# Kernel optimization log

Hardware: AMD Instinct MI355X
Metric: run time of the kernel (lower is better)

## Reference

```python
import jax, jax.numpy as jnp
import numpy as np

SIZE = 1024
SIZE_INTERNAL = 4096
B, S = 8, 2048
EPS = 1e-5


def layer_norm(x, g, b):
    mu = jnp.mean(x, axis=-1, keepdims=True)
    var = jnp.mean(jnp.square(x - mu), axis=-1, keepdims=True)
    return (x - mu) * jax.lax.rsqrt(var + EPS) * g + b


def setup_inputs() -> dict:
    key = jax.random.key(0)
    ks = jax.random.split(key, 12)
    s = 0.02
    return {
        "x": jax.random.normal(ks[0], (B, S, SIZE), jnp.float32),
        "Wq": jax.random.normal(ks[1], (SIZE, SIZE), jnp.float32) * s,
        "bq": jnp.zeros((SIZE,), jnp.float32),
        "Wk": jax.random.normal(ks[2], (SIZE, SIZE), jnp.float32) * s,
        "bk": jnp.zeros((SIZE,), jnp.float32),
        "Wv": jax.random.normal(ks[3], (SIZE, SIZE), jnp.float32) * s,
        "bv": jnp.zeros((SIZE,), jnp.float32),
        "W1": jax.random.normal(ks[4], (SIZE, SIZE_INTERNAL), jnp.float32) * s,
        "b1": jnp.zeros((SIZE_INTERNAL,), jnp.float32),
        "W2": jax.random.normal(ks[5], (SIZE_INTERNAL, SIZE), jnp.float32) * s,
        "b2": jnp.zeros((SIZE,), jnp.float32),
        "g1": jnp.ones((SIZE,), jnp.float32),
        "beta1": jnp.zeros((SIZE,), jnp.float32),
        "g2": jnp.ones((SIZE,), jnp.float32),
        "beta2": jnp.zeros((SIZE,), jnp.float32),
    }


def reference(x, Wq, bq, Wk, bk, Wv, bv, W1, b1, W2, b2, g1, beta1, g2, beta2):
    # QKV projections (single-head; bmm on 3D tensors in original)
    q = x @ Wq + bq  # (B,S,d)
    k = x @ Wk + bk
    v = x @ Wv + bv
    scale = 1.0 / jnp.sqrt(jnp.asarray(SIZE, x.dtype))
    scores = jnp.einsum("bqd,bkd->bqk", q, k) * scale  # (B,S,S)
    # decoder=True -> causal mask
    causal = jnp.tril(jnp.ones((S, S), bool))
    scores = jnp.where(causal, scores, jnp.asarray(-jnp.inf, x.dtype))
    attn = jax.nn.softmax(scores, axis=-1)
    attn_out = jnp.einsum("bqk,bkd->bqd", attn, v)
    attn_out = layer_norm(attn_out, g1, beta1)
    h = jax.nn.gelu(attn_out @ W1 + b1, approximate=False)
    out = h @ W2 + b2 + attn_out
    return layer_norm(out, g2, beta2)
```

## Files before the change

kernel.cpp:

```cpp
#include <hip/hip_runtime.h>
#include <cstdint>

#define DEV __device__ __forceinline__

typedef __attribute__((ext_vector_type(8))) short bf16x8;
typedef __attribute__((ext_vector_type(4))) float f32x4;
typedef unsigned short u16;
typedef unsigned int   u32;

DEV u16 f2bf(float f) {
  u32 u = __float_as_uint(f);
  u = (u + 0x7FFFu + ((u >> 16) & 1u)) >> 16;
  return (u16)u;
}
DEV float bf2f(u16 s) { return __uint_as_float(((u32)s) << 16); }

DEV float gelu_f(float x) {
  const float ax = fabsf(x) * 0.70710678118654752f;
  const float t = 1.f / fmaf(0.3275911f, ax, 1.f);
  float p = fmaf(1.061405429f, t, -1.453152027f);
  p = fmaf(p, t, 1.421413741f);
  p = fmaf(p, t, -0.284496736f);
  p = fmaf(p, t, 0.254829592f);
  p *= t;
  const float er = 1.f - p * __expf(-ax * ax);
  return 0.5f * x * (1.f + copysignf(er, x));
}

DEV void gload_lds16(const void* g, void* l) {
  typedef __attribute__((address_space(1))) const unsigned int GU;
  typedef __attribute__((address_space(3))) unsigned int LU;
  __builtin_amdgcn_global_load_lds((GU*)(uintptr_t)g, (LU*)(u32)(uintptr_t)l, 16, 0, 0);
}

DEV int swz(int x) { return x ^ (((x >> 7) & 7) << 4); }

#define BATCH_SC 2228224L

template<int MODE>
__global__ __launch_bounds__(256, 4)
void gemm_bt(const u16* __restrict__ A, int lda, long abst,
             const u16* __restrict__ Bt, int ldb, long bbst,
             void* __restrict__ Cv, int ldc, long cbst,
             const float* __restrict__ bias,
             const float* __restrict__ bias2,
             const float* __restrict__ bias3,
             int K, float scale)
{
  const int nt = blockIdx.x, mt = blockIdx.y, bz = blockIdx.z;
  if (MODE == 1 && nt > mt) return;
  const int Keff = (MODE == 2) ? (mt + 1) * 128 : K;

  __shared__ u16 As[128 * 64];
  __shared__ u16 Bs[128 * 64];

  const int tid  = threadIdx.x;
  const int lane = tid & 63;
  const int wv   = tid >> 6;
  const int wr   = wv >> 1, wc = wv & 1;
  const int lrow = lane & 15;
  const int kgrp = lane >> 4;
  const int m0 = mt * 128, n0 = nt * 128;

  const int srow = tid >> 3;
  const int scol = (tid & 7) * 8;
  const u16* Ag;
  if (MODE == 2) {
    Ag = A + bz * BATCH_SC + (long)(mt * (mt + 1) / 2) * 16384 + srow * 128 + scol;
  } else {
    Ag = A + (long)bz * abst + (long)(m0 + srow) * lda + scol;
  }
  const u16* Bg = Bt + (long)bz * bbst + (long)(n0 + srow) * ldb + scol;
  char* AsW = (char*)As + wv * 1024;
  char* BsW = (char*)Bs + wv * 1024;

  f32x4 acc[4][4];
#pragma unroll
  for (int mi = 0; mi < 4; ++mi)
#pragma unroll
    for (int ni = 0; ni < 4; ++ni)
#pragma unroll
      for (int e = 0; e < 4; ++e) acc[mi][ni][e] = 0.f;

  for (int k0 = 0; k0 < Keff; k0 += 64) {
#pragma unroll
    for (int i = 0; i < 4; ++i) {
      if (MODE == 2)
        gload_lds16(Ag + (long)(k0 >> 7) * 16384 + (k0 & 127) + i * 32 * 128, AsW + i * 4096);
      else
        gload_lds16(Ag + k0 + (long)i * 32 * lda, AsW + i * 4096);
      gload_lds16(Bg + k0 + (long)i * 32 * ldb, BsW + i * 4096);
    }
    __syncthreads();
#pragma unroll
    for (int kk = 0; kk < 2; ++kk) {
      const int kof = kk * 32 + kgrp * 8;
      bf16x8 af[4], bfr[4];
#pragma unroll
      for (int mi = 0; mi < 4; ++mi)
        af[mi] = *(const bf16x8*)&As[(wr * 64 + mi * 16 + lrow) * 64 + kof];
#pragma unroll
      for (int ni = 0; ni < 4; ++ni)
        bfr[ni] = *(const bf16x8*)&Bs[(wc * 64 + ni * 16 + lrow) * 64 + kof];
#pragma unroll
      for (int mi = 0; mi < 4; ++mi)
#pragma unroll
        for (int ni = 0; ni < 4; ++ni)
          acc[mi][ni] = __builtin_amdgcn_mfma_f32_16x16x32_bf16(af[mi], bfr[ni], acc[mi][ni], 0, 0, 0);
    }
    __syncthreads();
  }

#pragma unroll
  for (int mi = 0; mi < 4; ++mi) {
#pragma unroll
    for (int ni = 0; ni < 4; ++ni) {
#pragma unroll
      for (int e = 0; e < 4; ++e) {
        const int rr = wr * 64 + mi * 16 + kgrp * 4 + e;
        const int cc = wc * 64 + ni * 16 + lrow;
        const int gr = m0 + rr, gc = n0 + cc;
        const float v = acc[mi][ni][e];
        if (MODE == 0) {
          const float bval = gc < 1024 ? bias[gc]
                              : (gc < 2048 ? bias2[gc & 1023] : bias3[gc & 1023]);
          ((u16*)Cv)[(long)(gc >> 10) * 16777216 + (long)gr * 1024 + (gc & 1023)]
              = f2bf(v + bval);
        } else if (MODE == 1) {
          ((u16*)Cv)[bz * BATCH_SC + (long)(mt * (mt + 1) / 2 + nt) * 16384 + rr * 128 + cc]
              = f2bf(v * scale);
        } else if (MODE == 2) {
          ((u16*)Cv)[(long)bz * cbst + (long)gr * ldc + gc] = f2bf(v);
        } else if (MODE == 3) {
          ((u16*)Cv)[(long)gr * ldc + gc] = f2bf(gelu_f(v + bias[gc]));
        }
      }
    }
  }
}

template<int PASS>
__global__ __launch_bounds__(512, 2)
void gemm256_p8_ffn2(const u16* __restrict__ A, int lda,
                     const u16* __restrict__ Bt, int ldb,
                     float* __restrict__ Cv, int ldc,
                     const float* __restrict__ bias,
                     const u16* __restrict__ resid,
                     int K, int NNT)
{
  __shared__ char smem[131072];
  const int tid  = threadIdx.x;
  const int lane = tid & 63;
  const int wv   = tid >> 6;
  const int wm   = wv >> 2, wn = wv & 3;
  const int lrow = lane & 15;
  const int kgrp = lane >> 4;

  const int nwg = gridDim.x;
  const int q0 = nwg >> 3, r = nwg & 7, xc = blockIdx.x & 7, pos = blockIdx.x >> 3;
  const int s = (xc < r ? xc * (q0 + 1) : r * (q0 + 1) + (xc - r) * q0) + pos;
  const int mt = s / NNT, nt = s % NNT;
  const int m0 = mt * 256, n0 = nt * 256;

  auto stageA = [&](int ktile, int dslot, int h) {
    int k0 = ktile << 6; const int kmax = K - 64; if (k0 > kmax) k0 = kmax;
#pragma unroll
    for (int j = 0; j < 2; ++j) {
      const int o = j * 8192 + tid * 16;
      const int l = swz(o);
      gload_lds16(A + (long)(m0 + h * 128 + (l >> 7)) * lda + k0 + ((l & 127) >> 1),
                  smem + dslot * 65536 + h * 16384 + o);
    }
  };
  auto stageB = [&](int ktile, int dslot, int h) {
    int k0 = ktile << 6; const int kmax = K - 64; if (k0 > kmax) k0 = kmax;
#pragma unroll
    for (int j = 0; j < 2; ++j) {
      const int o = j * 8192 + tid * 16;
      const int l = swz(o);
      gload_lds16(Bt + (long)(n0 + h * 128 + (l >> 7)) * ldb + k0 + ((l & 127) >> 1),
                  smem + dslot * 65536 + 32768 + h * 16384 + o);
    }
  };
  auto rdfrag = [&](int bofs, int row, int ks) -> bf16x8 {
    const int p = swz(row * 128 + ks * 64 + kgrp * 16);
    return *(const bf16x8*)(smem + bofs + p);
  };

  f32x4 acc[8][4];
#pragma unroll
  for (int mi = 0; mi < 8; ++mi)
#pragma unroll
    for (int ni = 0; ni < 4; ++ni)
#pragma unroll
      for (int e = 0; e < 4; ++e) acc[mi][ni][e] = 0.f;

  stageA(0, 0, 0); stageA(0, 0, 1); stageB(0, 0, 0); stageB(0, 0, 1);
  stageB(1, 1, 0); stageB(1, 1, 1);
  asm volatile("s_waitcnt vmcnt(4)" ::: "memory");
  __builtin_amdgcn_s_barrier();

  const int NI = K >> 7;
  bf16x8 bfrag[4][2], afrag[2][2];
  for (int i = 0; i < NI; ++i) {
    const int kp = 2 * i;
#pragma unroll
    for (int d = 0; d < 2; ++d) {
#pragma unroll
      for (int mq = 0; mq < 4; ++mq) {
        const int ph = d * 4 + mq;
        if (mq == 0) {
#pragma unroll
          for (int ni = 0; ni < 4; ++ni)
#pragma unroll
            for (int ks = 0; ks < 2; ++ks)
              bfrag[ni][ks] = rdfrag(d * 65536 + 32768, wn * 64 + ni * 16 + lrow, ks);
        }
#pragma unroll
        for (int mi2 = 0; mi2 < 2; ++mi2)
#pragma unroll
          for (int ks = 0; ks < 2; ++ks)
            afrag[mi2][ks] = rdfrag(d * 65536, wm * 128 + (2 * mq + mi2) * 16 + lrow, ks);
        switch (ph) {
          case 0: stageA(kp + 1, 1, 0); break;
          case 1: stageA(kp + 1, 1, 1); break;
          case 2: stageB(kp + 2, 0, 0); break;
          case 3: stageB(kp + 2, 0, 1); break;
          case 4: stageA(kp + 2, 0, 0); break;
          case 5: stageA(kp + 2, 0, 1); break;
          case 6: stageB(kp + 3, 1, 0); break;
          case 7: stageB(kp + 3, 1, 1); break;
        }
        __builtin_amdgcn_s_barrier();
        asm volatile("s_waitcnt lgkmcnt(0)" ::: "memory");
        __builtin_amdgcn_s_setprio(1);
#pragma unroll
        for (int mi2 = 0; mi2 < 2; ++mi2)
#pragma unroll
          for (int ni = 0; ni < 4; ++ni)
#pragma unroll
            for (int ks = 0; ks < 2; ++ks)
              acc[2 * mq + mi2][ni] = __builtin_amdgcn_mfma_f32_16x16x32_bf16(
                  afrag[mi2][ks], bfrag[ni][ks], acc[2 * mq + mi2][ni], 0, 0, 0);
        __builtin_amdgcn_s_setprio(0);
        if (mq == 3) asm volatile("s_waitcnt vmcnt(4)" ::: "memory");
        __builtin_amdgcn_s_barrier();
      }
    }
  }

#pragma unroll
  for (int mi = 0; mi < 8; ++mi) {
#pragma unroll
    for (int ni = 0; ni < 4; ++ni) {
      const int gc = n0 + wn * 64 + ni * 16 + lrow;
#pragma unroll
      for (int e = 0; e < 4; ++e) {
        const int gr = m0 + wm * 128 + mi * 16 + kgrp * 4 + e;
        if (PASS == 0) {
          Cv[(long)gr * ldc + gc] = acc[mi][ni][e];
        } else if (PASS == 1) {
          float* o = &Cv[(long)gr * ldc + gc];
          *o = *o + acc[mi][ni][e] + bias[gc] + bf2f(resid[(long)gr * 1024 + gc]);
        } else {
          Cv[(long)gr * ldc + gc] = acc[mi][ni][e] + bias[gc]
                                    + bf2f(resid[(long)gr * 1024 + gc]);
        }
      }
    }
  }
}

template<int INBF>
__global__ __launch_bounds__(256)
void transpose_bf16(const void* __restrict__ inv, u16* __restrict__ out,
                    int R, int C, long ibst, long obst)
{
  __shared__ float t[32][33];
  const int bz = blockIdx.z;
  const int c0 = blockIdx.x * 32, r0 = blockIdx.y * 32;
  const int tx = threadIdx.x & 31, ty = threadIdx.x >> 5;
#pragma unroll
  for (int i = 0; i < 32; i += 8) {
    const long idx = (long)bz * ibst + (long)(r0 + ty + i) * C + (c0 + tx);
    t[ty + i][tx] = INBF ? bf2f(((const u16*)inv)[idx]) : ((const float*)inv)[idx];
  }
  __syncthreads();
#pragma unroll
  for (int i = 0; i < 32; i += 8)
    out[(long)bz * obst + (long)(c0 + ty + i) * R + (r0 + tx)] = f2bf(t[tx][ty + i]);
}

__global__ __launch_bounds__(256)
void cvt_f32_to_bf16(const float* __restrict__ in, u16* __restrict__ out, long n)
{
  const long idx = ((long)blockIdx.x * 256 + threadIdx.x) * 4;
  if (idx >= n) return;
  const float4 v = *(const float4*)(in + idx);
  ushort4 o;
  o.x = f2bf(v.x); o.y = f2bf(v.y); o.z = f2bf(v.z); o.w = f2bf(v.w);
  *(ushort4*)(out + idx) = o;
}

__global__ __launch_bounds__(256)
void softmax_packed(u16* __restrict__ sc)
{
  const int rowid = blockIdx.x;
  const int b = rowid >> 11, i = rowid & 2047;
  const int mtt = i >> 7, rr = i & 127;
  u16* base = sc + (long)b * BATCH_SC + (long)(mtt * (mtt + 1) / 2) * 16384 + (long)rr * 128;
  const int t = threadIdx.x;
  const int lane = t & 63, wv = t >> 6;
  const int c   = t >> 4;
  const int off = (t & 15) * 8;
  const bool act = (c <= mtt);
  const int lim = (c < mtt) ? 8 : (c == mtt ? (rr - off + 1) : 0);
  u16* p = base + (long)c * 16384 + off;

  bf16x8 vv = {};
  if (act) vv = *(const bf16x8*)p;
  float vals[8];
  float m = -1e30f;
#pragma unroll
  for (int e = 0; e < 8; ++e) {
    vals[e] = (e < lim) ? bf2f((u16)vv[e]) : -1e30f;
    m = fmaxf(m, vals[e]);
  }
#pragma unroll
  for (int o = 1; o < 64; o <<= 1) m = fmaxf(m, __shfl_xor(m, o));
  __shared__ float rm[4], rsm[4];
  if (lane == 0) rm[wv] = m;
  __syncthreads();
  m = fmaxf(fmaxf(rm[0], rm[1]), fmaxf(rm[2], rm[3]));
  float pv[8];
  float ssum = 0.f;
#pragma unroll
  for (int e = 0; e < 8; ++e) { pv[e] = __expf(vals[e] - m); ssum += pv[e]; }
#pragma unroll
  for (int o = 1; o < 64; o <<= 1) ssum += __shfl_xor(ssum, o);
  if (lane == 0) rsm[wv] = ssum;
  __syncthreads();
  ssum = rsm[0] + rsm[1] + rsm[2] + rsm[3];
  const float inv = 1.f / ssum;
  if (act) {
    bf16x8 o;
#pragma unroll
    for (int e = 0; e < 8; ++e) o[e] = (short)f2bf(pv[e] * inv);
    *(bf16x8*)p = o;
  }
}

template<int INBF, int OUTBF>
__global__ __launch_bounds__(256)
void layernorm_k(const void* __restrict__ in, const float* __restrict__ gam,
                 const float* __restrict__ bet, void* __restrict__ outv)
{
  const long row = blockIdx.x;
  const int t = threadIdx.x;
  const int lane = t & 63, wv = t >> 6;
  float v0, v1, v2, v3;
  if (INBF) {
    const ushort4 u = ((const ushort4*)in)[row * 256 + t];
    v0 = bf2f(u.x); v1 = bf2f(u.y); v2 = bf2f(u.z); v3 = bf2f(u.w);
  } else {
    const float4 v = ((const float4*)in)[row * 256 + t];
    v0 = v.x; v1 = v.y; v2 = v.z; v3 = v.w;
  }
  float s = v0 + v1 + v2 + v3;
  float q = v0 * v0 + v1 * v1 + v2 * v2 + v3 * v3;
#pragma unroll
  for (int o = 1; o < 64; o <<= 1) { s += __shfl_xor(s, o); q += __shfl_xor(q, o); }
  __shared__ float rs[4], rq[4];
  if (lane == 0) { rs[wv] = s; rq[wv] = q; }
  __syncthreads();
  s = rs[0] + rs[1] + rs[2] + rs[3];
  q = rq[0] + rq[1] + rq[2] + rq[3];
  const float mean = s * (1.f / 1024.f);
  const float var  = q * (1.f / 1024.f) - mean * mean;
  const float rstd = rsqrtf(var + 1e-5f);
  const float4 g4 = ((const float4*)gam)[t];
  const float4 b4 = ((const float4*)bet)[t];
  const float o0 = (v0 - mean) * rstd * g4.x + b4.x;
  const float o1 = (v1 - mean) * rstd * g4.y + b4.y;
  const float o2 = (v2 - mean) * rstd * g4.z + b4.z;
  const float o3 = (v3 - mean) * rstd * g4.w + b4.w;
  if (OUTBF) {
    ushort4 o; o.x = f2bf(o0); o.y = f2bf(o1); o.z = f2bf(o2); o.w = f2bf(o3);
    ((ushort4*)outv)[row * 256 + t] = o;
  } else {
    ((float4*)outv)[row * 256 + t] = make_float4(o0, o1, o2, o3);
  }
}

extern "C" void kernel_launch(void* const* d_in, const int* in_sizes, int n_in,
                              void* d_out, int out_size, void* d_ws, size_t ws_size,
                              hipStream_t stream)
{
  const float* x   = (const float*)d_in[0];
  const float* Wq  = (const float*)d_in[1];
  const float* bq  = (const float*)d_in[2];
  const float* Wk  = (const float*)d_in[3];
  const float* bk  = (const float*)d_in[4];
  const float* Wv  = (const float*)d_in[5];
  const float* bv  = (const float*)d_in[6];
  const float* W1  = (const float*)d_in[7];
  const float* b1  = (const float*)d_in[8];
  const float* W2  = (const float*)d_in[9];
  const float* b2  = (const float*)d_in[10];
  const float* g1  = (const float*)d_in[11];
  const float* be1 = (const float*)d_in[12];
  const float* g2  = (const float*)d_in[13];
  const float* be2 = (const float*)d_in[14];

  char* ws = (char*)d_ws;
  u16*   wqkvT = (u16*)(ws);
  u16*   w1T   = (u16*)(ws + 6291456);
  u16*   w2T   = (u16*)(ws + 14680064);
  u16*   xb    = (u16*)(ws + 23068672);
  u16*   vt    = xb;
  u16*   qkv   = (u16*)(ws + 56623104);
  u16*   qbuf  = qkv;
  u16*   kbuf  = qkv + 16777216;
  u16*   vbuf  = qkv + 33554432;
  u16*   ln1   = qbuf;
  u16*   pvout = kbuf;
  u16*   sc    = (u16*)(ws + 123731968);
  u16*   hbuf  = kbuf;
  const bool big = (ws_size >= 224395264ULL);

  const dim3 B256(256);

  cvt_f32_to_bf16<<<dim3(16384), B256, 0, stream>>>(x, xb, 16777216L);

  transpose_bf16<0><<<dim3(32, 32, 1),  B256, 0, stream>>>(Wq, wqkvT,           1024, 1024, 0, 0);
  transpose_bf16<0><<<dim3(32, 32, 1),  B256, 0, stream>>>(Wk, wqkvT + 1048576, 1024, 1024, 0, 0);
  transpose_bf16<0><<<dim3(32, 32, 1),  B256, 0, stream>>>(Wv, wqkvT + 2097152, 1024, 1024, 0, 0);
  transpose_bf16<0><<<dim3(128, 32, 1), B256, 0, stream>>>(W1, w1T, 1024, 4096, 0, 0);
  transpose_bf16<0><<<dim3(32, 128, 1), B256, 0, stream>>>(W2, w2T, 4096, 1024, 0, 0);

  gemm_bt<0><<<dim3(24, 128), B256, 0, stream>>>(xb, 1024, 0, wqkvT, 1024, 0, qkv, 1024, 0,
                                                 bq, bk, bv, 1024, 1.f);

  transpose_bf16<1><<<dim3(32, 64, 8), B256, 0, stream>>>(vbuf, vt, 2048, 1024, 2097152, 2097152);

  gemm_bt<1><<<dim3(16, 16, 8), B256, 0, stream>>>(qbuf, 1024, 2097152, kbuf, 1024, 2097152,
                                                   sc, 0, 0, nullptr, nullptr, nullptr,
                                                   1024, 0.03125f);

  softmax_packed<<<dim3(16384), B256, 0, stream>>>(sc);

  gemm_bt<2><<<dim3(8, 16, 8), B256, 0, stream>>>(sc, 0, 0, vt, 2048, 2097152,
                                                  pvout, 1024, 2097152, nullptr, nullptr, nullptr,
                                                  0, 1.f);

  layernorm_k<1, 1><<<dim3(16384), B256, 0, stream>>>(pvout, g1, be1, ln1);

  if (big) {
    gemm_bt<3><<<dim3(32, 128), B256, 0, stream>>>(ln1, 1024, 0, w1T, 1024, 0, hbuf, 4096, 0,
                                                   b1, nullptr, nullptr, 1024, 1.f);
    gemm256_p8_ffn2<2><<<dim3(256), dim3(512), 0, stream>>>(hbuf, 4096, w2T, 4096,
                                                            (float*)d_out, 1024,
                                                            b2, ln1, 4096, 4);
  } else {
    for (int j = 0; j < 2; ++j) {
      const u16* w1h = w1T + (long)j * 2048 * 1024;
      gemm_bt<3><<<dim3(16, 128), B256, 0, stream>>>(ln1, 1024, 0, w1h, 1024, 0, hbuf, 2048, 0,
                                                     b1 + j * 2048, nullptr, nullptr, 1024, 1.f);
      if (j == 0)
        gemm256_p8_ffn2<0><<<dim3(256), dim3(512), 0, stream>>>(hbuf, 2048, w2T, 4096,
                                                                (float*)d_out, 1024,
                                                                nullptr, nullptr, 2048, 4);
      else
        gemm256_p8_ffn2<1><<<dim3(256), dim3(512), 0, stream>>>(hbuf, 2048, w2T + 2048, 4096,
                                                                (float*)d_out, 1024,
                                                                b2, ln1, 2048, 4);
    }
  }

  layernorm_k<0, 0><<<dim3(16384), B256, 0, stream>>>(d_out, g2, be2, d_out);
}
```

Measured before the change: 692.3 us.

## Approximate GELU with sigmoid, merge weight transposes, bf16 FFN2 output

Replaces the erf-based GELU polynomial with a cheaper exp2/sigmoid-style approximation in the FFN1 epilogue. Merges the five weight transpose launches into a single prep_weights kernel to cut launch overhead. In the big-workspace path, FFN2 writes a bf16 intermediate instead of fp32 and the final layernorm reads bf16, reducing memory traffic. The sigmoid GELU approximation and the bf16 rounding before layernorm both reduce accuracy.

```diff
diff --git a/kernel.cpp b/kernel.cpp
--- a/kernel.cpp
+++ b/kernel.cpp
@@ -16,15 +16,10 @@
 DEV float bf2f(u16 s) { return __uint_as_float(((u32)s) << 16); }
 
 DEV float gelu_f(float x) {
-  const float ax = fabsf(x) * 0.70710678118654752f;
-  const float t = 1.f / fmaf(0.3275911f, ax, 1.f);
-  float p = fmaf(1.061405429f, t, -1.453152027f);
-  p = fmaf(p, t, 1.421413741f);
-  p = fmaf(p, t, -0.284496736f);
-  p = fmaf(p, t, 0.254829592f);
-  p *= t;
-  const float er = 1.f - p * __expf(-ax * ax);
-  return 0.5f * x * (1.f + copysignf(er, x));
+  const float x2 = x * x;
+  const float z  = x * fmaf(-0.1029436f, x2, -2.3022082f);
+  const float e  = exp2f(z);
+  return x * (1.f / (1.f + e));
 }
 
 DEV void gload_lds16(const void* g, void* l) {
@@ -143,7 +138,7 @@
 __global__ __launch_bounds__(512, 2)
 void gemm256_p8_ffn2(const u16* __restrict__ A, int lda,
                      const u16* __restrict__ Bt, int ldb,
-                     float* __restrict__ Cv, int ldc,
+                     void* __restrict__ Cv, int ldc,
                      const float* __restrict__ bias,
                      const u16* __restrict__ resid,
                      int K, int NNT)
@@ -258,23 +253,52 @@
       for (int e = 0; e < 4; ++e) {
         const int gr = m0 + wm * 128 + mi * 16 + kgrp * 4 + e;
         if (PASS == 0) {
-          Cv[(long)gr * ldc + gc] = acc[mi][ni][e];
+          ((float*)Cv)[(long)gr * ldc + gc] = acc[mi][ni][e];
         } else if (PASS == 1) {
-          float* o = &Cv[(long)gr * ldc + gc];
+          float* o = &((float*)Cv)[(long)gr * ldc + gc];
           *o = *o + acc[mi][ni][e] + bias[gc] + bf2f(resid[(long)gr * 1024 + gc]);
         } else {
-          Cv[(long)gr * ldc + gc] = acc[mi][ni][e] + bias[gc]
-                                    + bf2f(resid[(long)gr * 1024 + gc]);
+          ((u16*)Cv)[(long)gr * ldc + gc]
+              = f2bf(acc[mi][ni][e] + bias[gc] + bf2f(resid[(long)gr * 1024 + gc]));
         }
       }
     }
   }
 }
 
-template<int INBF>
 __global__ __launch_bounds__(256)
-void transpose_bf16(const void* __restrict__ inv, u16* __restrict__ out,
-                    int R, int C, long ibst, long obst)
+void prep_weights(const float* __restrict__ Wq, const float* __restrict__ Wk,
+                  const float* __restrict__ Wv, const float* __restrict__ W1,
+                  const float* __restrict__ W2,
+                  u16* __restrict__ wqkvT, u16* __restrict__ w1T, u16* __restrict__ w2T)
+{
+  const int idx = blockIdx.x;
+  const float* in; u16* out; int R, C, cx0, ry0;
+  if (idx < 3072) {
+    in = (idx < 1024) ? Wq : (idx < 2048 ? Wk : Wv);
+    out = wqkvT + (long)(idx >> 10) * 1048576;
+    const int i = idx & 1023; cx0 = (i & 31) * 32; ry0 = (i >> 5) * 32; R = 1024; C = 1024;
+  } else if (idx < 7168) {
+    const int i = idx - 3072; in = W1; out = w1T; R = 1024; C = 4096;
+    cx0 = (i & 127) * 32; ry0 = (i >> 7) * 32;
+  } else {
+    const int i = idx - 7168; in = W2; out = w2T; R = 4096; C = 1024;
+    cx0 = (i & 31) * 32; ry0 = (i >> 5) * 32;
+  }
+  __shared__ float t[32][33];
+  const int tx = threadIdx.x & 31, ty = threadIdx.x >> 5;
+#pragma unroll
+  for (int i = 0; i < 32; i += 8)
+    t[ty + i][tx] = in[(long)(ry0 + ty + i) * C + (cx0 + tx)];
+  __syncthreads();
+#pragma unroll
+  for (int i = 0; i < 32; i += 8)
+    out[(long)(cx0 + ty + i) * R + (ry0 + tx)] = f2bf(t[tx][ty + i]);
+}
+
+__global__ __launch_bounds__(256)
+void transpose_v(const u16* __restrict__ inv, u16* __restrict__ out,
+                 int R, int C, long ibst, long obst)
 {
   __shared__ float t[32][33];
   const int bz = blockIdx.z;
@@ -283,7 +307,7 @@
 #pragma unroll
   for (int i = 0; i < 32; i += 8) {
     const long idx = (long)bz * ibst + (long)(r0 + ty + i) * C + (c0 + tx);
-    t[ty + i][tx] = INBF ? bf2f(((const u16*)inv)[idx]) : ((const float*)inv)[idx];
+    t[ty + i][tx] = bf2f(inv[idx]);
   }
   __syncthreads();
 #pragma unroll
@@ -418,6 +442,7 @@
   u16*   w2T   = (u16*)(ws + 14680064);
   u16*   xb    = (u16*)(ws + 23068672);
   u16*   vt    = xb;
+  u16*   f2out = xb;
   u16*   qkv   = (u16*)(ws + 56623104);
   u16*   qbuf  = qkv;
   u16*   kbuf  = qkv + 16777216;
@@ -432,16 +457,12 @@
 
   cvt_f32_to_bf16<<<dim3(16384), B256, 0, stream>>>(x, xb, 16777216L);
 
-  transpose_bf16<0><<<dim3(32, 32, 1),  B256, 0, stream>>>(Wq, wqkvT,           1024, 1024, 0, 0);
-  transpose_bf16<0><<<dim3(32, 32, 1),  B256, 0, stream>>>(Wk, wqkvT + 1048576, 1024, 1024, 0, 0);
-  transpose_bf16<0><<<dim3(32, 32, 1),  B256, 0, stream>>>(Wv, wqkvT + 2097152, 1024, 1024, 0, 0);
-  transpose_bf16<0><<<dim3(128, 32, 1), B256, 0, stream>>>(W1, w1T, 1024, 4096, 0, 0);
-  transpose_bf16<0><<<dim3(32, 128, 1), B256, 0, stream>>>(W2, w2T, 4096, 1024, 0, 0);
+  prep_weights<<<dim3(11264), B256, 0, stream>>>(Wq, Wk, Wv, W1, W2, wqkvT, w1T, w2T);
 
   gemm_bt<0><<<dim3(24, 128), B256, 0, stream>>>(xb, 1024, 0, wqkvT, 1024, 0, qkv, 1024, 0,
                                                  bq, bk, bv, 1024, 1.f);
 
-  transpose_bf16<1><<<dim3(32, 64, 8), B256, 0, stream>>>(vbuf, vt, 2048, 1024, 2097152, 2097152);
+  transpose_v<<<dim3(32, 64, 8), B256, 0, stream>>>(vbuf, vt, 2048, 1024, 2097152, 2097152);
 
   gemm_bt<1><<<dim3(16, 16, 8), B256, 0, stream>>>(qbuf, 1024, 2097152, kbuf, 1024, 2097152,
                                                    sc, 0, 0, nullptr, nullptr, nullptr,
@@ -459,8 +480,8 @@
     gemm_bt<3><<<dim3(32, 128), B256, 0, stream>>>(ln1, 1024, 0, w1T, 1024, 0, hbuf, 4096, 0,
                                                    b1, nullptr, nullptr, 1024, 1.f);
     gemm256_p8_ffn2<2><<<dim3(256), dim3(512), 0, stream>>>(hbuf, 4096, w2T, 4096,
-                                                            (float*)d_out, 1024,
-                                                            b2, ln1, 4096, 4);
+                                                            f2out, 1024, b2, ln1, 4096, 4);
+    layernorm_k<1, 0><<<dim3(16384), B256, 0, stream>>>(f2out, g2, be2, d_out);
   } else {
     for (int j = 0; j < 2; ++j) {
       const u16* w1h = w1T + (long)j * 2048 * 1024;
@@ -468,14 +489,13 @@
                                                      b1 + j * 2048, nullptr, nullptr, 1024, 1.f);
       if (j == 0)
         gemm256_p8_ffn2<0><<<dim3(256), dim3(512), 0, stream>>>(hbuf, 2048, w2T, 4096,
-                                                                (float*)d_out, 1024,
+                                                                d_out, 1024,
                                                                 nullptr, nullptr, 2048, 4);
       else
         gemm256_p8_ffn2<1><<<dim3(256), dim3(512), 0, stream>>>(hbuf, 2048, w2T + 2048, 4096,
-                                                                (float*)d_out, 1024,
+                                                                d_out, 1024,
                                                                 b2, ln1, 2048, 4);
     }
-  }
-
-  layernorm_k<0, 0><<<dim3(16384), B256, 0, stream>>>(d_out, g2, be2, d_out);
-}
+    layernorm_k<0, 0><<<dim3(16384), B256, 0, stream>>>(d_out, g2, be2, d_out);
+  }
+}
```

Result: faster. 663.7 us (-4.1%).
